# Optimization experiments

Measured on AMD Instinct MI355X. Metric: run time of the kernel, lower is better.

Reference implementation:

```python
import jax, jax.numpy as jnp
import numpy as np

N_NODES = 50000
N_EDGES = 500000
F_IN = 128
F_OUT = 128
N_REL = 8


def setup_inputs() -> dict:
    key = jax.random.key(0)
    ks = jax.random.split(key, 10)
    x = jax.random.normal(ks[0], (N_NODES, F_IN), dtype=jnp.float32)
    edge_index = jax.random.randint(ks[1], (2, N_EDGES), 0, N_NODES, dtype=jnp.int64)
    edge_types = jax.random.randint(ks[2], (N_EDGES,), 0, N_REL, dtype=jnp.int64)
    s = 1.0 / np.sqrt(F_IN)
    Wr = jax.random.uniform(ks[3], (N_REL, F_OUT, F_IN), jnp.float32, -s, s)  # per-relation Linear weights [out,in]
    br = jax.random.uniform(ks[4], (N_REL, F_OUT), jnp.float32, -s, s)
    Ws = jax.random.uniform(ks[5], (F_OUT, F_IN), jnp.float32, -s, s)         # self Linear
    bs = jax.random.uniform(ks[6], (F_OUT,), jnp.float32, -s, s)
    sa = 1.0 / np.sqrt(2 * F_IN)
    wa = jax.random.uniform(ks[7], (2 * F_IN,), jnp.float32, -sa, sa)         # attention Linear(2*in, 1) weight
    ba = jax.random.uniform(ks[8], (1,), jnp.float32, -sa, sa)
    return {"x": x, "edge_index": edge_index, "edge_types": edge_types,
            "Wr": Wr, "br": br, "Ws": Ws, "bs": bs, "wa": wa, "ba": ba}


def reference(x, edge_index, edge_types, Wr, br, Ws, bs, wa, ba):
    N, Fin = x.shape
    R = Wr.shape[0]
    src, tgt = edge_index[0], edge_index[1]
    # self term: self_weight(x)
    out = x @ Ws.T + bs
    # attention: sigmoid(cat(x[src], x[tgt]) @ wa + ba), decomposed per node then gathered
    a_src = x @ wa[:Fin]   # [N]
    a_tgt = x @ wa[Fin:]   # [N]
    a = jax.nn.sigmoid(a_src[src] + a_tgt[tgt] + ba[0])  # [E]
    # contribution per edge: a * (x[src] @ Wr^T + br)  =>  aggregate (a * x[src]) and a per (target, relation)
    scaled = x[src] * a[:, None]                         # [E, Fin]
    seg = tgt * R + edge_types                           # combined (target, relation) segment id
    agg = jax.ops.segment_sum(scaled, seg, num_segments=N * R).reshape(N, R, Fin)
    asum = jax.ops.segment_sum(a, seg, num_segments=N * R).reshape(N, R)
    out = out + jnp.einsum('nri,roi->no', agg, Wr) + asum @ br
    return out
```

## Files before the change

kernel.cpp:

```cpp
#include <hip/hip_runtime.h>
#include <math.h>

#define NND 50000
#define NED 500000
#define FDIM 128
#define NREL 8
#define NSL 9
#define MPAD 50048
#define CAP 64

typedef __attribute__((ext_vector_type(8))) short short8;
typedef __attribute__((ext_vector_type(4))) float f32x4;
typedef const void __attribute__((address_space(1)))* gptr_t;
typedef void __attribute__((address_space(3)))* lptr_t;

static __device__ __forceinline__ unsigned short f2bf(float f) {
    unsigned u = __float_as_uint(f);
    u += 0x7FFFu + ((u >> 16) & 1u);
    return (unsigned short)(u >> 16);
}
static __device__ __forceinline__ float bf2f(unsigned short b) {
    return __uint_as_float((unsigned)b << 16);
}

#define NDB   12500
#define XZB   3
#define PBB   72
#define CZB   196
__global__ void node_dots_kernel(const float* __restrict__ x,
                                 const float* __restrict__ wa,
                                 float* __restrict__ a_src,
                                 float* __restrict__ a_tgt,
                                 unsigned short* __restrict__ xb,
                                 const float* __restrict__ Ws,
                                 const float* __restrict__ Wr,
                                 unsigned short* __restrict__ Bt2,
                                 int* __restrict__ counts) {
    int b = blockIdx.x;
    if (b < NDB) {
        int gid  = b * 256 + threadIdx.x;
        int node = gid >> 6;
        int lane = threadIdx.x & 63;
        float2 v = *(const float2*)(x + (size_t)node * FDIM + lane * 2);
        ushort2 vb = { f2bf(v.x), f2bf(v.y) };
        *(ushort2*)(xb + (size_t)node * FDIM + lane * 2) = vb;
        float s1 = v.x * wa[2 * lane]        + v.y * wa[2 * lane + 1];
        float s2 = v.x * wa[FDIM + 2 * lane] + v.y * wa[FDIM + 2 * lane + 1];
#pragma unroll
        for (int off = 32; off > 0; off >>= 1) {
            s1 += __shfl_xor(s1, off);
            s2 += __shfl_xor(s2, off);
        }
        if (lane == 0) { a_src[node] = s1; a_tgt[node] = s2; }
    } else if (b < NDB + XZB) {
        int i = (b - NDB) * 256 + threadIdx.x;
        float4 z = make_float4(0.f, 0.f, 0.f, 0.f);
        ((float4*)(xb + (size_t)NND * FDIM))[i] = z;
    } else if (b < NDB + XZB + PBB) {
        int idx0 = (b - NDB - XZB) * 2048 + threadIdx.x * 8;
        int o2 = idx0 >> 7;
        int k0 = idx0 & 127;
        int s  = o2 >> 7;
        int o  = o2 & 127;
        unsigned short tmp[8];
#pragma unroll
        for (int j = 0; j < 8; ++j) {
            int k = k0 + j;
            float v = (s == 0) ? Ws[o * FDIM + k]
                               : Wr[(((size_t)(s - 1) * FDIM) + o) * FDIM + k];
            tmp[j] = f2bf(v);
        }
        *(short8*)(Bt2 + idx0) = *(short8*)tmp;
    } else {
        int i = (b - NDB - XZB - PBB) * 256 + threadIdx.x;
        if (i < NND) counts[i] = 0;
    }
}

__global__ void scatter_kernel(const int* __restrict__ ei, const int* __restrict__ et,
                               const float* __restrict__ a_src, const float* __restrict__ a_tgt,
                               const float* __restrict__ ba,
                               int* __restrict__ counts,
                               unsigned long long* __restrict__ sorted2) {
    int e = blockIdx.x * blockDim.x + threadIdx.x;
    if (e >= NED) return;
    int src = ei[e];
    int tgt = ei[NED + e];
    int rel = et[e];
    float s = a_src[src] + a_tgt[tgt] + ba[0];
    float a = 1.0f / (1.0f + __expf(-s));
    int slot = atomicAdd(&counts[tgt], 1);
    if (slot < CAP) {
        unsigned long long pk = ((unsigned long long)__float_as_uint(a) << 32)
                              | (unsigned)((rel << 16) | src);
        sorted2[(size_t)tgt * CAP + slot] = pk;
    }
}

__global__ __launch_bounds__(256) void gemm_z_kernel(
        const unsigned short* __restrict__ xb,
        const unsigned short* __restrict__ Bt2,
        const float* __restrict__ br,
        const float* __restrict__ bs,
        unsigned short* __restrict__ Z,
        float* __restrict__ out) {
    __shared__ __align__(16) unsigned short AsB[64 * 64];
    __shared__ __align__(16) unsigned short BsB[128 * 64];
    int tid  = threadIdx.x;
    int wave = tid >> 6;
    int lane = tid & 63;
    int l15  = lane & 15;
    int lhi  = lane >> 4;
    int bid  = blockIdx.x;
    int mtile = bid / NSL;
    int slice = bid - mtile * NSL;
    int brow = mtile * 64;
    int wr = wave >> 1;
    int wc = wave & 1;

    f32x4 acc[2][4];
#pragma unroll
    for (int mi = 0; mi < 2; ++mi)
#pragma unroll
        for (int ni = 0; ni < 4; ++ni) acc[mi][ni] = (f32x4){0.f, 0.f, 0.f, 0.f};

    for (int kc = 0; kc < 2; ++kc) {
#pragma unroll
        for (int q = 0; q < 2; ++q) {
            int c    = tid + q * 256;
            int trow = c >> 3;
            int csw  = (c & 7) ^ (trow & 7);
            const unsigned short* src = xb + (size_t)(brow + trow) * FDIM + kc * 64 + csw * 8;
            __builtin_amdgcn_global_load_lds((gptr_t)src,
                (lptr_t)&AsB[wave * 512 + q * 2048], 16, 0, 0);
        }
#pragma unroll
        for (int q = 0; q < 4; ++q) {
            int c   = tid + q * 256;
            int o   = c >> 3;
            int csw = (c & 7) ^ (o & 7);
            const unsigned short* src = Bt2 + ((size_t)slice * FDIM + o) * FDIM + kc * 64 + csw * 8;
            __builtin_amdgcn_global_load_lds((gptr_t)src,
                (lptr_t)&BsB[wave * 512 + q * 2048], 16, 0, 0);
        }
        __syncthreads();
#pragma unroll
        for (int ks = 0; ks < 2; ++ks) {
            int kslot = ks * 4 + lhi;
            short8 a[2], b[4];
#pragma unroll
            for (int mi = 0; mi < 2; ++mi) {
                int row = wr * 32 + mi * 16 + l15;
                a[mi] = *(const short8*)&AsB[row * 64 + ((kslot ^ (row & 7)) << 3)];
            }
#pragma unroll
            for (int ni = 0; ni < 4; ++ni) {
                int o = wc * 64 + ni * 16 + l15;
                b[ni] = *(const short8*)&BsB[o * 64 + ((kslot ^ (o & 7)) << 3)];
            }
#pragma unroll
            for (int mi = 0; mi < 2; ++mi)
#pragma unroll
                for (int ni = 0; ni < 4; ++ni)
                    acc[mi][ni] = __builtin_amdgcn_mfma_f32_16x16x32_bf16(
                        a[mi], b[ni], acc[mi][ni], 0, 0, 0);
        }
        __syncthreads();
    }

    if (slice == 0) {
#pragma unroll
        for (int mi = 0; mi < 2; ++mi) {
            int rowbase = brow + wr * 32 + mi * 16 + lhi * 4;
#pragma unroll
            for (int j = 0; j < 4; ++j) {
                int row = rowbase + j;
                if (row >= NND) continue;
#pragma unroll
                for (int ni = 0; ni < 4; ++ni) {
                    int col = wc * 64 + ni * 16 + l15;
                    out[(size_t)row * FDIM + col] = acc[mi][ni][j] + bs[col];
                }
            }
        }
    } else {
        const float* brr = br + (size_t)(slice - 1) * FDIM;
        unsigned short* zb = Z + (size_t)(slice - 1) * FDIM;
#pragma unroll
        for (int mi = 0; mi < 2; ++mi) {
            int rowbase = brow + wr * 32 + mi * 16 + lhi * 4;
#pragma unroll
            for (int j = 0; j < 4; ++j) {
                int row = rowbase + j;
#pragma unroll
                for (int ni = 0; ni < 4; ++ni) {
                    int col = wc * 64 + ni * 16 + l15;
                    zb[(size_t)row * (NREL * FDIM) + col] = f2bf(acc[mi][ni][j] + brr[col]);
                }
            }
        }
    }
}

__global__ __launch_bounds__(256) void edge_agg_kernel(
        const int* __restrict__ counts, const unsigned long long* __restrict__ sorted2,
        const unsigned short* __restrict__ Z,
        float* __restrict__ out) {
    int wid  = (blockIdx.x * blockDim.x + threadIdx.x) >> 6;
    int lane = threadIdx.x & 63;
    if (wid >= NND) return;
    int tgt = wid;
    int cnt = counts[tgt];
    if (cnt > CAP) cnt = CAP;
    const unsigned long long* seg = sorted2 + (size_t)tgt * CAP;

    float2 c = {0.f, 0.f};
    const ushort2* zl = (const ushort2*)Z + lane;

#define ZIDX(PK) ((size_t)((((PK) & 0xFFFFu) << 3) | (((PK) >> 16) & 7u)) * 64)

    for (int base = 0; base < cnt; base += 16) {
        unsigned long long pk[16];
#pragma unroll
        for (int j = 0; j < 16; ++j)
            pk[j] = (base + j < cnt) ? seg[base + j] : 0ull;
        ushort2 w[16];
#pragma unroll
        for (int j = 0; j < 16; ++j)
            w[j] = zl[ZIDX(pk[j])];
#pragma unroll
        for (int j = 0; j < 16; ++j) {
            float a = __uint_as_float((unsigned)(pk[j] >> 32));
            c.x += a * bf2f(w[j].x);
            c.y += a * bf2f(w[j].y);
        }
    }
#undef ZIDX

    float2* op = (float2*)(out + (size_t)tgt * FDIM) + lane;
    float2 v = *op;
    v.x += c.x;
    v.y += c.y;
    *op = v;
}

extern "C" void kernel_launch(void* const* d_in, const int* in_sizes, int n_in,
                              void* d_out, int out_size, void* d_ws, size_t ws_size,
                              hipStream_t stream) {
    const float* x  = (const float*)d_in[0];
    const int*   ei = (const int*)d_in[1];
    const int*   et = (const int*)d_in[2];
    const float* Wr = (const float*)d_in[3];
    const float* br = (const float*)d_in[4];
    const float* Ws = (const float*)d_in[5];
    const float* bs = (const float*)d_in[6];
    const float* wa = (const float*)d_in[7];
    const float* ba = (const float*)d_in[8];
    float* out = (float*)d_out;
    float* ws  = (float*)d_ws;

    const size_t xbF  = ((size_t)MPAD * FDIM) / 2;
    const size_t btF  = ((size_t)NSL * FDIM * FDIM) / 2;
    const size_t zF   = ((size_t)MPAD * NREL * FDIM) / 2;
    size_t o = 0;
    unsigned short* xb  = (unsigned short*)(ws + o); o += xbF;
    unsigned short* Bt2 = (unsigned short*)(ws + o); o += btF;
    unsigned short* Z   = (unsigned short*)(ws + o); o += zF;
    float* a_src = ws + o; o += NND;
    float* a_tgt = ws + o; o += NND;
    int*   counts = (int*)(ws + o); o += NND;
    unsigned long long* sorted2 = (unsigned long long*)(ws + o); o += 2 * (size_t)NND * CAP;
    if (ws_size < o * sizeof(float)) return;

    dim3 blk(256);

    node_dots_kernel<<<NDB + XZB + PBB + CZB, blk, 0, stream>>>(
        x, wa, a_src, a_tgt, xb, Ws, Wr, Bt2, counts);
    scatter_kernel<<<(NED + 255) / 256, blk, 0, stream>>>(
        ei, et, a_src, a_tgt, ba, counts, sorted2);
    gemm_z_kernel<<<(MPAD / 64) * NSL, blk, 0, stream>>>(xb, Bt2, br, bs, Z, out);
    edge_agg_kernel<<<(NND + 3) / 4, blk, 0, stream>>>(counts, sorted2, Z, out);
}
```

Before: 111.7 us.

## Merge scatter into GEMM launch and process two targets per wave in aggregation

Folds the edge scatter kernel into the GEMM kernel as extra leading blocks, so the independent scatter and Z GEMM work share one launch and can overlap on the GPU. The edge aggregation kernel now has each half-wave handle one target node and read 8-byte ushort4 vectors of Z instead of 4-byte ushort2. This is meant to cut launch overhead and idle gaps and to raise memory-level parallelism in the gather. In exchange, both halves of a wave loop to the larger of their two edge counts, which adds divergence. The merged kernel also carries the GEMM's shared memory footprint into the scatter blocks.

```diff
diff --git a/kernel.cpp b/kernel.cpp
--- a/kernel.cpp
+++ b/kernel.cpp
@@ -8,6 +8,8 @@
 #define NSL 9
 #define MPAD 50048
 #define CAP 64
+#define SCB 1954
+#define GZB ((MPAD / 64) * NSL)
 
 typedef __attribute__((ext_vector_type(8))) short short8;
 typedef __attribute__((ext_vector_type(4))) float f32x4;
@@ -77,27 +79,12 @@
     }
 }
 
-__global__ void scatter_kernel(const int* __restrict__ ei, const int* __restrict__ et,
-                               const float* __restrict__ a_src, const float* __restrict__ a_tgt,
-                               const float* __restrict__ ba,
-                               int* __restrict__ counts,
-                               unsigned long long* __restrict__ sorted2) {
-    int e = blockIdx.x * blockDim.x + threadIdx.x;
-    if (e >= NED) return;
-    int src = ei[e];
-    int tgt = ei[NED + e];
-    int rel = et[e];
-    float s = a_src[src] + a_tgt[tgt] + ba[0];
-    float a = 1.0f / (1.0f + __expf(-s));
-    int slot = atomicAdd(&counts[tgt], 1);
-    if (slot < CAP) {
-        unsigned long long pk = ((unsigned long long)__float_as_uint(a) << 32)
-                              | (unsigned)((rel << 16) | src);
-        sorted2[(size_t)tgt * CAP + slot] = pk;
-    }
-}
-
-__global__ __launch_bounds__(256) void gemm_z_kernel(
+__global__ __launch_bounds__(256) void gemm_scatter_kernel(
+        const int* __restrict__ ei, const int* __restrict__ et,
+        const float* __restrict__ a_src, const float* __restrict__ a_tgt,
+        const float* __restrict__ ba,
+        int* __restrict__ counts,
+        unsigned long long* __restrict__ sorted2,
         const unsigned short* __restrict__ xb,
         const unsigned short* __restrict__ Bt2,
         const float* __restrict__ br,
@@ -106,12 +93,30 @@
         float* __restrict__ out) {
     __shared__ __align__(16) unsigned short AsB[64 * 64];
     __shared__ __align__(16) unsigned short BsB[128 * 64];
+
+    if (blockIdx.x < SCB) {
+        int e = blockIdx.x * 256 + threadIdx.x;
+        if (e >= NED) return;
+        int src = ei[e];
+        int tgt = ei[NED + e];
+        int rel = et[e];
+        float s = a_src[src] + a_tgt[tgt] + ba[0];
+        float a = 1.0f / (1.0f + __expf(-s));
+        int slot = atomicAdd(&counts[tgt], 1);
+        if (slot < CAP) {
+            unsigned long long pk = ((unsigned long long)__float_as_uint(a) << 32)
+                                  | (unsigned)((rel << 16) | src);
+            sorted2[(size_t)tgt * CAP + slot] = pk;
+        }
+        return;
+    }
+
     int tid  = threadIdx.x;
     int wave = tid >> 6;
     int lane = tid & 63;
     int l15  = lane & 15;
     int lhi  = lane >> 4;
-    int bid  = blockIdx.x;
+    int bid  = blockIdx.x - SCB;
     int mtile = bid / NSL;
     int slice = bid - mtile * NSL;
     int brow = mtile * 64;
@@ -208,39 +213,40 @@
         float* __restrict__ out) {
     int wid  = (blockIdx.x * blockDim.x + threadIdx.x) >> 6;
     int lane = threadIdx.x & 63;
-    if (wid >= NND) return;
-    int tgt = wid;
+    if (wid >= NND / 2) return;
+    int h   = lane >> 5;
+    int hl  = lane & 31;
+    int tgt = wid * 2 + h;
     int cnt = counts[tgt];
     if (cnt > CAP) cnt = CAP;
+    int cntm = max(cnt, __shfl_xor(cnt, 32));
     const unsigned long long* seg = sorted2 + (size_t)tgt * CAP;
-
-    float2 c = {0.f, 0.f};
-    const ushort2* zl = (const ushort2*)Z + lane;
-
-#define ZIDX(PK) ((size_t)((((PK) & 0xFFFFu) << 3) | (((PK) >> 16) & 7u)) * 64)
-
-    for (int base = 0; base < cnt; base += 16) {
-        unsigned long long pk[16];
-#pragma unroll
-        for (int j = 0; j < 16; ++j)
+    const ushort4* zl = (const ushort4*)Z + hl;
+
+    float4 c = make_float4(0.f, 0.f, 0.f, 0.f);
+
+    for (int base = 0; base < cntm; base += 8) {
+        unsigned long long pk[8];
+#pragma unroll
+        for (int j = 0; j < 8; ++j)
             pk[j] = (base + j < cnt) ? seg[base + j] : 0ull;
-        ushort2 w[16];
-#pragma unroll
-        for (int j = 0; j < 16; ++j)
-            w[j] = zl[ZIDX(pk[j])];
-#pragma unroll
-        for (int j = 0; j < 16; ++j) {
+        ushort4 w[8];
+#pragma unroll
+        for (int j = 0; j < 8; ++j)
+            w[j] = zl[(size_t)((((pk[j] & 0xFFFFu) << 3) | ((pk[j] >> 16) & 7u))) * 32];
+#pragma unroll
+        for (int j = 0; j < 8; ++j) {
             float a = __uint_as_float((unsigned)(pk[j] >> 32));
             c.x += a * bf2f(w[j].x);
             c.y += a * bf2f(w[j].y);
-        }
-    }
-#undef ZIDX
-
-    float2* op = (float2*)(out + (size_t)tgt * FDIM) + lane;
-    float2 v = *op;
-    v.x += c.x;
-    v.y += c.y;
+            c.z += a * bf2f(w[j].z);
+            c.w += a * bf2f(w[j].w);
+        }
+    }
+
+    float4* op = (float4*)(out + (size_t)tgt * FDIM) + hl;
+    float4 v = *op;
+    v.x += c.x; v.y += c.y; v.z += c.z; v.w += c.w;
     *op = v;
 }
 
@@ -276,8 +282,7 @@
 
     node_dots_kernel<<<NDB + XZB + PBB + CZB, blk, 0, stream>>>(
         x, wa, a_src, a_tgt, xb, Ws, Wr, Bt2, counts);
-    scatter_kernel<<<(NED + 255) / 256, blk, 0, stream>>>(
-        ei, et, a_src, a_tgt, ba, counts, sorted2);
-    gemm_z_kernel<<<(MPAD / 64) * NSL, blk, 0, stream>>>(xb, Bt2, br, bs, Z, out);
-    edge_agg_kernel<<<(NND + 3) / 4, blk, 0, stream>>>(counts, sorted2, Z, out);
-}
+    gemm_scatter_kernel<<<SCB + GZB, blk, 0, stream>>>(
+        ei, et, a_src, a_tgt, ba, counts, sorted2, xb, Bt2, br, bs, Z, out);
+    edge_agg_kernel<<<(NND / 2 + 3) / 4, blk, 0, stream>>>(counts, sorted2, Z, out);
+}
```

After: 106.1 us. 1.05x faster.
